# Performance work log

Measured on AMD Instinct MI355X. Metric: run time of the kernel, lower is better.

## Reference

```python
import jax, jax.numpy as jnp
import numpy as np
import math

D_MODEL = 1024
NUM_HEADS = 16
D_K = D_MODEL // NUM_HEADS
B, S = 2, 2048


def setup_inputs() -> dict:
    key = jax.random.key(0)
    ks = jax.random.split(key, 11)
    scale = 1.0 / math.sqrt(D_MODEL)
    inp = {
        "query": jax.random.normal(ks[0], (B, S, D_MODEL), jnp.float32),
        "key": jax.random.normal(ks[1], (B, S, D_MODEL), jnp.float32),
        "value": jax.random.normal(ks[2], (B, S, D_MODEL), jnp.float32),
        "Wq": jax.random.normal(ks[3], (D_MODEL, D_MODEL), jnp.float32) * scale,
        "bq": jnp.zeros((D_MODEL,), jnp.float32),
        "Wk": jax.random.normal(ks[4], (D_MODEL, D_MODEL), jnp.float32) * scale,
        "bk": jnp.zeros((D_MODEL,), jnp.float32),
        "Wv": jax.random.normal(ks[5], (D_MODEL, D_MODEL), jnp.float32) * scale,
        "bv": jnp.zeros((D_MODEL,), jnp.float32),
        "Wo": jax.random.normal(ks[6], (D_MODEL, D_MODEL), jnp.float32) * scale,
        "bo": jnp.zeros((D_MODEL,), jnp.float32),
    }
    return inp


def reference(query, key, value, Wq, bq, Wk, bk, Wv, bv, Wo, bo):
    b, s, _ = query.shape
    # QKV projections (torch Linear: x @ W.T + b)
    Q = query @ Wq.T + bq
    K = key @ Wk.T + bk
    V = value @ Wv.T + bv
    # [b, h, s, d_k]
    Q = Q.reshape(b, s, NUM_HEADS, D_K).transpose(0, 2, 1, 3)
    K = K.reshape(b, s, NUM_HEADS, D_K).transpose(0, 2, 1, 3)
    V = V.reshape(b, s, NUM_HEADS, D_K).transpose(0, 2, 1, 3)
    score = jnp.einsum("bhqd,bhkd->bhqk", Q, K) / math.sqrt(D_K)
    attn = jax.nn.softmax(score, axis=-1)
    out = jnp.einsum("bhqk,bhkd->bhqd", attn, V)
    out = out.transpose(0, 2, 1, 3).reshape(b, s, D_MODEL)
    return out @ Wo.T + bo
```

## Files before the change

### kernel.cpp

```cpp
#include <hip/hip_runtime.h>

#define NHEADS 16
#define SEQ    2048
#define BATCH  2
#define DMODEL 1024
#define MTOT   4096

typedef __attribute__((ext_vector_type(8)))  short short8;
typedef __attribute__((ext_vector_type(4)))  float f32x4;
typedef __attribute__((ext_vector_type(16))) float f32x16;

__device__ __forceinline__ unsigned short f32_to_bf16_rn(float x) {
  unsigned int u = __float_as_uint(x);
  u += 0x7fffu + ((u >> 16) & 1u);
  return (unsigned short)(u >> 16);
}

__device__ __forceinline__ unsigned cvt_pk_bf16(float lo, float hi_) {
  unsigned r;
  asm("v_cvt_pk_bf16_f32 %0, %1, %2" : "=v"(r) : "v"(lo), "v"(hi_));
  return r;
}

__device__ __forceinline__ void permlane32_swap(unsigned &a, unsigned &b) {
  asm("v_permlane32_swap_b32 %0, %1" : "+v"(a), "+v"(b));
}

__device__ __forceinline__ void async16(void* lds, const void* g) {
  __builtin_amdgcn_global_load_lds((const __attribute__((address_space(1))) unsigned int*)g,
                                   (__attribute__((address_space(3))) unsigned int*)lds, 16, 0, 0);
}

__global__ void cvt_bf16_kernel(const float* __restrict__ x0, const float* __restrict__ x1,
                                const float* __restrict__ x2,
                                const float* __restrict__ w0, const float* __restrict__ w1,
                                const float* __restrict__ w2, const float* __restrict__ w3,
                                unsigned short* __restrict__ obase)
{
  const int e = (blockIdx.x*256 + threadIdx.x)*8;
  const float* src;
  int local;
  if (e < 3*4194304) {
    const int t = e >> 22;
    src = t==0 ? x0 : t==1 ? x1 : x2;
    local = e & (4194304-1);
    src += local;
    local += t << 22;
  } else {
    const int f = e - 3*4194304;
    const int t = f >> 20;
    src = t==0 ? w0 : t==1 ? w1 : t==2 ? w2 : w3;
    src += (f & (1048576-1));
    local = e;
  }
  const float4 v0 = *(const float4*)(src);
  const float4 v1 = *(const float4*)(src + 4);
  union { unsigned short u[8]; uint4 v; } r;
  r.u[0] = f32_to_bf16_rn(v0.x); r.u[1] = f32_to_bf16_rn(v0.y);
  r.u[2] = f32_to_bf16_rn(v0.z); r.u[3] = f32_to_bf16_rn(v0.w);
  r.u[4] = f32_to_bf16_rn(v1.x); r.u[5] = f32_to_bf16_rn(v1.y);
  r.u[6] = f32_to_bf16_rn(v1.z); r.u[7] = f32_to_bf16_rn(v1.w);
  *(uint4*)(obase + local) = r.v;
}

template<int BM>
__device__ __forceinline__ void gemm_core(const unsigned short* __restrict__ A,
                                          const unsigned short* __restrict__ W,
                                          unsigned short* sA, unsigned short* sB,
                                          int m0, int n0, f32x4 (&acc)[BM/32][4])
{
  constexpr int MI = BM/32;
  const int t = threadIdx.x;
  const int lane = t & 63;
  const int wv = t >> 6;
  const int wm = wv >> 1, wn = wv & 1;
  const int lr = lane & 15, lk = lane >> 4;

  for (int kt = 0; kt < DMODEL/64; ++kt) {
    #pragma unroll
    for (int g = 0; g < MI; ++g) {
      const int o  = g*4096 + t*16;
      const int so = o ^ (((o >> 7) & 7) << 4);
      const int row = so >> 7, colE = (so & 127) >> 1;
      async16((char*)sA + o, A + (size_t)(m0 + row)*DMODEL + kt*64 + colE);
    }
    #pragma unroll
    for (int g = 0; g < 4; ++g) {
      const int o  = g*4096 + t*16;
      const int so = o ^ (((o >> 7) & 7) << 4);
      const int row = so >> 7, colE = (so & 127) >> 1;
      async16((char*)sB + o, W + (size_t)(n0 + row)*DMODEL + kt*64 + colE);
    }
    __syncthreads();
    #pragma unroll
    for (int ks = 0; ks < 2; ++ks) {
      short8 af[MI], bf[4];
      #pragma unroll
      for (int mi = 0; mi < MI; ++mi) {
        const int row = wm*(BM/2) + mi*16 + lr;
        const int sl  = (ks*4 + lk) ^ (row & 7);
        af[mi] = *(const short8*)(sA + row*64 + sl*8);
      }
      #pragma unroll
      for (int ni = 0; ni < 4; ++ni) {
        const int row = wn*64 + ni*16 + lr;
        const int sl  = (ks*4 + lk) ^ (row & 7);
        bf[ni] = *(const short8*)(sB + row*64 + sl*8);
      }
      #pragma unroll
      for (int mi = 0; mi < MI; ++mi)
        #pragma unroll
        for (int ni = 0; ni < 4; ++ni)
          acc[mi][ni] = __builtin_amdgcn_mfma_f32_16x16x32_bf16(af[mi], bf[ni], acc[mi][ni], 0, 0, 0);
    }
    __syncthreads();
  }
}

__global__ __launch_bounds__(256, 3)
void qkv_gemm_kernel(const unsigned short* __restrict__ Xq, const unsigned short* __restrict__ Xk,
                     const unsigned short* __restrict__ Xv,
                     const unsigned short* __restrict__ Wq, const unsigned short* __restrict__ Wk,
                     const unsigned short* __restrict__ Wv,
                     const float* __restrict__ bq, const float* __restrict__ bk,
                     const float* __restrict__ bv,
                     unsigned short* __restrict__ Qp, unsigned short* __restrict__ Kp,
                     unsigned short* __restrict__ Vtp)
{
  constexpr int BM = 128;
  constexpr int MI = BM/32;
  __shared__ __align__(16) unsigned short smem[17024];
  unsigned short* sA = smem;
  unsigned short* sB = smem + 8192;

  const int m0   = blockIdx.x * BM;
  const int nabs = blockIdx.y * 128;
  const int wsel = nabs >> 10;
  const int n0   = nabs & 1023;
  const unsigned short* A = wsel==0 ? Xq : wsel==1 ? Xk : Xv;
  const unsigned short* W = wsel==0 ? Wq : wsel==1 ? Wk : Wv;
  const float* bias       = wsel==0 ? bq : wsel==1 ? bk : bv;

  f32x4 acc[MI][4];
  #pragma unroll
  for (int mi = 0; mi < MI; ++mi)
    #pragma unroll
    for (int ni = 0; ni < 4; ++ni)
      acc[mi][ni] = {0.f, 0.f, 0.f, 0.f};

  gemm_core<BM>(A, W, sA, sB, m0, n0, acc);

  const int t = threadIdx.x, lane = t & 63, wvx = t >> 6;
  const int wm = wvx >> 1, wn = wvx & 1;
  const int lr = lane & 15, lk = lane >> 4;

  if (wsel == 2) {
    #pragma unroll
    for (int ni = 0; ni < 4; ++ni) {
      const float badd = bias[n0 + wn*64 + ni*16 + lr];
      #pragma unroll
      for (int mi = 0; mi < MI; ++mi)
        #pragma unroll
        for (int r = 0; r < 4; ++r) {
          const int ml = wm*(BM/2) + mi*16 + lk*4 + r;
          smem[(wn*64 + ni*16 + lr)*132 + ml] = f32_to_bf16_rn(acc[mi][ni][r] + badd);
        }
    }
    __syncthreads();
    const int bb = m0 >> 11, s0 = m0 & 2047;
    const int jr = (t & 15)*8, nr = t >> 4;
    #pragma unroll
    for (int pass = 0; pass < 8; ++pass) {
      const int n  = pass*16 + nr;
      const int nn = n0 + n, hh = nn >> 6, d = nn & 63;
      const short8 v = *(const short8*)(smem + n*132 + jr);
      *(short8*)(Vtp + (((size_t)bb*NHEADS + hh)*64 + d)*SEQ + s0 + jr) = v;
    }
  } else {
    unsigned short* dst = wsel==0 ? Qp : Kp;
    const float qscale = (wsel == 0) ? 0.125f * 1.4426950408889634f : 1.0f;
    #pragma unroll
    for (int ni = 0; ni < 4; ++ni) {
      const int nn = n0 + wn*64 + ni*16 + lr;
      const float badd = bias[nn];
      const int hh = nn >> 6, d = nn & 63;
      #pragma unroll
      for (int mi = 0; mi < MI; ++mi) {
        #pragma unroll
        for (int r = 0; r < 4; ++r) {
          const int m = m0 + wm*(BM/2) + mi*16 + lk*4 + r;
          const int bb = m >> 11, s = m & 2047;
          const float v = (acc[mi][ni][r] + badd) * qscale;
          dst[(((size_t)bb*NHEADS + hh)*SEQ + s)*64 + d] = f32_to_bf16_rn(v);
        }
      }
    }
  }
}

__global__ __launch_bounds__(256, 2)
void attn_kernel(const unsigned short* __restrict__ Qp, const unsigned short* __restrict__ Kp,
                 const unsigned short* __restrict__ Vtp,
                 unsigned short* __restrict__ Opar, float* __restrict__ Lpar)
{
  __shared__ __align__(16) unsigned short sm[16384];
  constexpr int NT = 1024/64;

  const int t = threadIdx.x, lane = t & 63, w = t >> 6;
  const int lq = lane & 31, hi = lane >> 5;
  const int f   = blockIdx.x;
  const int wid = (f & 7)*64 + (f >> 3);
  const int qt = wid & 7, h = (wid >> 3) & 15, b = (wid >> 7) & 1, half = (wid >> 8) & 1;

  const size_t bh = (size_t)b*NHEADS + h;
  const unsigned short* Qh = Qp  + bh*SEQ*64;
  const unsigned short* Kh = Kp  + bh*SEQ*64 + (size_t)half*1024*64;
  const unsigned short* Vh = Vtp + bh*64*SEQ;
  const int q0 = qt*256 + w*64;

  short8 qf[2][4];
  #pragma unroll
  for (int qh = 0; qh < 2; ++qh)
    #pragma unroll
    for (int ks = 0; ks < 4; ++ks)
      qf[qh][ks] = *(const short8*)(Qh + (size_t)(q0 + qh*32 + lq)*64 + ks*16 + hi*8);

  f32x16 z16;
  #pragma unroll
  for (int r = 0; r < 16; ++r) z16[r] = 0.f;

  const unsigned short* srcp0;
  size_t sstride;
  if (w < 2) { srcp0 = Kh + (size_t)(w*32 + lq)*64 + hi*8;                      sstride = 64*64; }
  else       { srcp0 = Vh + (size_t)((w-2)*32 + lq)*2048 + half*1024 + hi*8;    sstride = 64;    }

  #pragma unroll
  for (int i = 0; i < 4; ++i)
    async16((char*)sm + w*4096 + i*1024, srcp0 + i*16);

  f32x16 o[2][2];
  float lsa[2][4];
  #pragma unroll
  for (int qh = 0; qh < 2; ++qh) {
    #pragma unroll
    for (int d = 0; d < 2; ++d)
      #pragma unroll
      for (int r = 0; r < 16; ++r) o[qh][d][r] = 0.f;
    #pragma unroll
    for (int j = 0; j < 4; ++j) lsa[qh][j] = 0.f;
  }

  for (int kt = 0; kt < NT; ++kt) {
    {
      const unsigned short* sp = srcp0 + (size_t)((kt + 1) & (NT - 1))*sstride;
      const int nb = ((kt + 1) & 1) * 16384;
      #pragma unroll
      for (int i = 0; i < 4; ++i)
        async16((char*)sm + nb + w*4096 + i*1024, sp + i*16);
    }
    asm volatile("s_waitcnt vmcnt(4)" ::: "memory");
    __builtin_amdgcn_s_barrier();

    const unsigned short* base  = sm + (kt & 1)*8192;
    const unsigned short* vbase = base + 4096;

    f32x16 st[2][2];
    __builtin_amdgcn_s_setprio(1);
    #pragma unroll
    for (int sub = 0; sub < 2; ++sub) {
      #pragma unroll
      for (int ks = 0; ks < 4; ++ks) {
        const short8 kf = *(const short8*)(base + (sub*4 + ks)*512 + lane*8);
        if (ks == 0) {
          st[0][sub] = __builtin_amdgcn_mfma_f32_32x32x16_bf16(kf, qf[0][0], z16, 0, 0, 0);
          st[1][sub] = __builtin_amdgcn_mfma_f32_32x32x16_bf16(kf, qf[1][0], z16, 0, 0, 0);
        } else {
          st[0][sub] = __builtin_amdgcn_mfma_f32_32x32x16_bf16(kf, qf[0][ks], st[0][sub], 0, 0, 0);
          st[1][sub] = __builtin_amdgcn_mfma_f32_32x32x16_bf16(kf, qf[1][ks], st[1][sub], 0, 0, 0);
        }
      }
    }
    __builtin_amdgcn_s_setprio(0);

    unsigned pw[2][2][8];
    #pragma unroll
    for (int qh = 0; qh < 2; ++qh)
      #pragma unroll
      for (int sub = 0; sub < 2; ++sub) {
        #pragma unroll
        for (int r = 0; r < 16; ++r) {
          const float p = __builtin_amdgcn_exp2f(st[qh][sub][r]);
          st[qh][sub][r] = p;
          lsa[qh][r & 3] += p;
        }
        unsigned x0 = cvt_pk_bf16(st[qh][sub][0],  st[qh][sub][1]);
        unsigned x1 = cvt_pk_bf16(st[qh][sub][2],  st[qh][sub][3]);
        unsigned y0 = cvt_pk_bf16(st[qh][sub][4],  st[qh][sub][5]);
        unsigned y1 = cvt_pk_bf16(st[qh][sub][6],  st[qh][sub][7]);
        permlane32_swap(x0, y0);
        permlane32_swap(x1, y1);
        pw[qh][sub][0] = x0; pw[qh][sub][1] = x1; pw[qh][sub][2] = y0; pw[qh][sub][3] = y1;
        unsigned z0 = cvt_pk_bf16(st[qh][sub][8],  st[qh][sub][9]);
        unsigned z1 = cvt_pk_bf16(st[qh][sub][10], st[qh][sub][11]);
        unsigned w0 = cvt_pk_bf16(st[qh][sub][12], st[qh][sub][13]);
        unsigned w1 = cvt_pk_bf16(st[qh][sub][14], st[qh][sub][15]);
        permlane32_swap(z0, w0);
        permlane32_swap(z1, w1);
        pw[qh][sub][4] = z0; pw[qh][sub][5] = z1; pw[qh][sub][6] = w0; pw[qh][sub][7] = w1;
      }

    #pragma unroll
    for (int sub = 0; sub < 2; ++sub) {
      const short8 v00 = *(const short8*)(vbase + (0*4 + 2*sub    )*512 + lane*8);
      const short8 v01 = *(const short8*)(vbase + (0*4 + 2*sub + 1)*512 + lane*8);
      const short8 v10 = *(const short8*)(vbase + (1*4 + 2*sub    )*512 + lane*8);
      const short8 v11 = *(const short8*)(vbase + (1*4 + 2*sub + 1)*512 + lane*8);
      __builtin_amdgcn_s_setprio(1);
      #pragma unroll
      for (int qh = 0; qh < 2; ++qh) {
        union { unsigned u[4]; short8 s; } pA, pB;
        pA.u[0] = pw[qh][sub][0]; pA.u[1] = pw[qh][sub][1];
        pA.u[2] = pw[qh][sub][2]; pA.u[3] = pw[qh][sub][3];
        pB.u[0] = pw[qh][sub][4]; pB.u[1] = pw[qh][sub][5];
        pB.u[2] = pw[qh][sub][6]; pB.u[3] = pw[qh][sub][7];
        o[qh][0] = __builtin_amdgcn_mfma_f32_32x32x16_bf16(v00, pA.s, o[qh][0], 0, 0, 0);
        o[qh][1] = __builtin_amdgcn_mfma_f32_32x32x16_bf16(v10, pA.s, o[qh][1], 0, 0, 0);
        o[qh][0] = __builtin_amdgcn_mfma_f32_32x32x16_bf16(v01, pB.s, o[qh][0], 0, 0, 0);
        o[qh][1] = __builtin_amdgcn_mfma_f32_32x32x16_bf16(v11, pB.s, o[qh][1], 0, 0, 0);
      }
      __builtin_amdgcn_s_setprio(0);
    }
    asm volatile("" ::: "memory");
    __builtin_amdgcn_s_barrier();
  }

  float lsum[2];
  #pragma unroll
  for (int qh = 0; qh < 2; ++qh) {
    lsum[qh] = (lsa[qh][0] + lsa[qh][1]) + (lsa[qh][2] + lsa[qh][3]);
    lsum[qh] += __shfl_xor(lsum[qh], 32);
  }
  if (lane < 32) {
    Lpar[half*65536 + b*32768 + h*2048 + q0 + lq]      = lsum[0];
    Lpar[half*65536 + b*32768 + h*2048 + q0 + 32 + lq] = lsum[1];
  }

  #pragma unroll
  for (int qh = 0; qh < 2; ++qh) {
    const size_t row = (size_t)b*SEQ + q0 + qh*32 + lq;
    unsigned short* orow = Opar + ((size_t)half*MTOT + row)*DMODEL + h*64;
    #pragma unroll
    for (int dblk = 0; dblk < 2; ++dblk)
      #pragma unroll
      for (int g = 0; g < 4; ++g) {
        union { unsigned short us[4]; uint2 v; } pk;
        #pragma unroll
        for (int r = 0; r < 4; ++r) pk.us[r] = f32_to_bf16_rn(o[qh][dblk][g*4 + r]);
        *(uint2*)(orow + dblk*32 + g*8 + hi*4) = pk.v;
      }
  }
}

__global__ void combine_kernel(const unsigned short* __restrict__ Opar,
                               const float* __restrict__ Lpar,
                               unsigned short* __restrict__ Op)
{
  const int flat = blockIdx.x*256 + threadIdx.x;
  const int row  = flat >> 8;
  const int col4 = flat & 255;
  const int b = row >> 11, q = row & 2047, h = col4 >> 4;

  const uint2 a = *(const uint2*)(Opar + (size_t)row*DMODEL + col4*4);
  const uint2 c = *(const uint2*)(Opar + (size_t)(MTOT + row)*DMODEL + col4*4);
  const float l0 = Lpar[b*32768 + h*2048 + q];
  const float l1 = Lpar[65536 + b*32768 + h*2048 + q];
  const float inv = __builtin_amdgcn_rcpf(l0 + l1);

  union { unsigned u[2]; uint2 v; } ua, uc;
  ua.v = a; uc.v = c;
  union { unsigned short us[4]; uint2 v; } out;
  #pragma unroll
  for (int j = 0; j < 4; ++j) {
    const unsigned va = ((j & 1) ? (ua.u[j >> 1] >> 16) : (ua.u[j >> 1] & 0xffffu)) << 16;
    const unsigned vc = ((j & 1) ? (uc.u[j >> 1] >> 16) : (uc.u[j >> 1] & 0xffffu)) << 16;
    const float s = (__uint_as_float(va) + __uint_as_float(vc)) * inv;
    out.us[j] = f32_to_bf16_rn(s);
  }
  *(uint2*)(Op + (size_t)row*DMODEL + col4*4) = out.v;
}

__global__ __launch_bounds__(256, 2)
void oproj_gemm_kernel(const unsigned short* __restrict__ Oin, const unsigned short* __restrict__ Wo,
                       const float* __restrict__ bo, float* __restrict__ out)
{
  constexpr int BM = 64;
  constexpr int MI = BM/32;
  __shared__ __align__(16) unsigned short sA[BM*64];
  __shared__ __align__(16) unsigned short sB[128*64];
  const int m0 = blockIdx.x * BM;
  const int n0 = blockIdx.y * 128;

  f32x4 acc[MI][4];
  #pragma unroll
  for (int mi = 0; mi < MI; ++mi)
    #pragma unroll
    for (int ni = 0; ni < 4; ++ni)
      acc[mi][ni] = {0.f,0.f,0.f,0.f};

  gemm_core<BM>(Oin, Wo, sA, sB, m0, n0, acc);

  const int t = threadIdx.x, lane = t & 63, wvx = t >> 6;
  const int wm = wvx >> 1, wn = wvx & 1;
  const int lr = lane & 15, lk = lane >> 4;

  #pragma unroll
  for (int ni = 0; ni < 4; ++ni) {
    const int nn = n0 + wn*64 + ni*16 + lr;
    const float badd = bo[nn];
    #pragma unroll
    for (int mi = 0; mi < MI; ++mi)
      #pragma unroll
      for (int r = 0; r < 4; ++r) {
        const int m = m0 + wm*(BM/2) + mi*16 + lk*4 + r;
        out[(size_t)m*DMODEL + nn] = acc[mi][ni][r] + badd;
      }
  }
}

extern "C" void kernel_launch(void* const* d_in, const int* in_sizes, int n_in,
                              void* d_out, int out_size, void* d_ws, size_t ws_size,
                              hipStream_t stream) {
  const float* query = (const float*)d_in[0];
  const float* key   = (const float*)d_in[1];
  const float* value = (const float*)d_in[2];
  const float* Wq    = (const float*)d_in[3];
  const float* bq    = (const float*)d_in[4];
  const float* Wk    = (const float*)d_in[5];
  const float* bk    = (const float*)d_in[6];
  const float* Wv    = (const float*)d_in[7];
  const float* bv    = (const float*)d_in[8];
  const float* Wo    = (const float*)d_in[9];
  const float* bo    = (const float*)d_in[10];

  const size_t NX = (size_t)MTOT*DMODEL;
  const size_t NW = (size_t)DMODEL*DMODEL;
  unsigned short* w   = (unsigned short*)d_ws;
  unsigned short* Xq  = w;
  unsigned short* Xk  = Xq  + NX;
  unsigned short* Xv  = Xk  + NX;
  unsigned short* Wqp = Xv  + NX;
  unsigned short* Wkp = Wqp + NW;
  unsigned short* Wvp = Wkp + NW;
  unsigned short* Wop = Wvp + NW;
  unsigned short* Qp  = Wop + NW;
  unsigned short* Kp  = Qp  + NX;
  unsigned short* Vtp = Kp  + NX;
  unsigned short* Opb = Vtp + NX;
  unsigned short* Opar = w;
  float*          Lpar = (float*)(w + 2*NX);

  cvt_bf16_kernel<<<dim3(8192), 256, 0, stream>>>(
      query, key, value, Wq, Wk, Wv, Wo, w);
  qkv_gemm_kernel<<<dim3(32, 24), 256, 0, stream>>>(
      Xq, Xk, Xv, Wqp, Wkp, Wvp, bq, bk, bv, Qp, Kp, Vtp);
  attn_kernel<<<dim3(512), 256, 0, stream>>>(Qp, Kp, Vtp, Opar, Lpar);
  combine_kernel<<<dim3(4096), 256, 0, stream>>>(Opar, Lpar, Opb);
  oproj_gemm_kernel<<<dim3(64, 8), 256, 0, stream>>>(Opb, Wop, bo, (float*)d_out);
}
```

Measured before the change: 118.1 us.

## Fuse split-KV combine into O-projection GEMM A-tile loading; drop setprio

```diff
diff --git a/kernel.cpp b/kernel.cpp
--- a/kernel.cpp
+++ b/kernel.cpp
@@ -265,7 +265,6 @@
     const unsigned short* vbase = base + 4096;
 
     f32x16 st[2][2];
-    __builtin_amdgcn_s_setprio(1);
     #pragma unroll
     for (int sub = 0; sub < 2; ++sub) {
       #pragma unroll
@@ -280,7 +279,6 @@
         }
       }
     }
-    __builtin_amdgcn_s_setprio(0);
 
     unsigned pw[2][2][8];
     #pragma unroll
@@ -315,7 +313,6 @@
       const short8 v01 = *(const short8*)(vbase + (0*4 + 2*sub + 1)*512 + lane*8);
       const short8 v10 = *(const short8*)(vbase + (1*4 + 2*sub    )*512 + lane*8);
       const short8 v11 = *(const short8*)(vbase + (1*4 + 2*sub + 1)*512 + lane*8);
-      __builtin_amdgcn_s_setprio(1);
       #pragma unroll
       for (int qh = 0; qh < 2; ++qh) {
         union { unsigned u[4]; short8 s; } pA, pB;
@@ -328,7 +325,6 @@
         o[qh][0] = __builtin_amdgcn_mfma_f32_32x32x16_bf16(v01, pB.s, o[qh][0], 0, 0, 0);
         o[qh][1] = __builtin_amdgcn_mfma_f32_32x32x16_bf16(v11, pB.s, o[qh][1], 0, 0, 0);
       }
-      __builtin_amdgcn_s_setprio(0);
     }
     asm volatile("" ::: "memory");
     __builtin_amdgcn_s_barrier();
@@ -361,36 +357,9 @@
   }
 }
 
-__global__ void combine_kernel(const unsigned short* __restrict__ Opar,
-                               const float* __restrict__ Lpar,
-                               unsigned short* __restrict__ Op)
-{
-  const int flat = blockIdx.x*256 + threadIdx.x;
-  const int row  = flat >> 8;
-  const int col4 = flat & 255;
-  const int b = row >> 11, q = row & 2047, h = col4 >> 4;
-
-  const uint2 a = *(const uint2*)(Opar + (size_t)row*DMODEL + col4*4);
-  const uint2 c = *(const uint2*)(Opar + (size_t)(MTOT + row)*DMODEL + col4*4);
-  const float l0 = Lpar[b*32768 + h*2048 + q];
-  const float l1 = Lpar[65536 + b*32768 + h*2048 + q];
-  const float inv = __builtin_amdgcn_rcpf(l0 + l1);
-
-  union { unsigned u[2]; uint2 v; } ua, uc;
-  ua.v = a; uc.v = c;
-  union { unsigned short us[4]; uint2 v; } out;
-  #pragma unroll
-  for (int j = 0; j < 4; ++j) {
-    const unsigned va = ((j & 1) ? (ua.u[j >> 1] >> 16) : (ua.u[j >> 1] & 0xffffu)) << 16;
-    const unsigned vc = ((j & 1) ? (uc.u[j >> 1] >> 16) : (uc.u[j >> 1] & 0xffffu)) << 16;
-    const float s = (__uint_as_float(va) + __uint_as_float(vc)) * inv;
-    out.us[j] = f32_to_bf16_rn(s);
-  }
-  *(uint2*)(Op + (size_t)row*DMODEL + col4*4) = out.v;
-}
-
 __global__ __launch_bounds__(256, 2)
-void oproj_gemm_kernel(const unsigned short* __restrict__ Oin, const unsigned short* __restrict__ Wo,
+void oproj_gemm_kernel(const unsigned short* __restrict__ Opar, const float* __restrict__ Lpar,
+                       const unsigned short* __restrict__ Wo,
                        const float* __restrict__ bo, float* __restrict__ out)
 {
   constexpr int BM = 64;
@@ -400,18 +369,72 @@
   const int m0 = blockIdx.x * BM;
   const int n0 = blockIdx.y * 128;
 
-  f32x4 acc[MI][4];
-  #pragma unroll
-  for (int mi = 0; mi < MI; ++mi)
-    #pragma unroll
-    for (int ni = 0; ni < 4; ++ni)
-      acc[mi][ni] = {0.f,0.f,0.f,0.f};
-
-  gemm_core<BM>(Oin, Wo, sA, sB, m0, n0, acc);
-
   const int t = threadIdx.x, lane = t & 63, wvx = t >> 6;
   const int wm = wvx >> 1, wn = wvx & 1;
   const int lr = lane & 15, lk = lane >> 4;
+
+  f32x4 acc[MI][4];
+  #pragma unroll
+  for (int mi = 0; mi < MI; ++mi)
+    #pragma unroll
+    for (int ni = 0; ni < 4; ++ni)
+      acc[mi][ni] = {0.f,0.f,0.f,0.f};
+
+  for (int kt = 0; kt < DMODEL/64; ++kt) {
+    #pragma unroll
+    for (int g = 0; g < MI; ++g) {
+      const int o  = g*4096 + t*16;
+      const int so = o ^ (((o >> 7) & 7) << 4);
+      const int row = so >> 7, colE = (so & 127) >> 1;
+      const int m = m0 + row, bb = m >> 11, q = m & 2047;
+      const uint4 a0 = *(const uint4*)(Opar + (size_t)m*DMODEL + kt*64 + colE);
+      const uint4 a1 = *(const uint4*)(Opar + (size_t)(MTOT + m)*DMODEL + kt*64 + colE);
+      const float l0 = Lpar[bb*32768 + kt*2048 + q];
+      const float l1 = Lpar[65536 + bb*32768 + kt*2048 + q];
+      const float inv = __builtin_amdgcn_rcpf(l0 + l1);
+      union { uint4 v; unsigned u[4]; } ua, ub, rs;
+      ua.v = a0; ub.v = a1;
+      #pragma unroll
+      for (int j = 0; j < 4; ++j) {
+        const float s0 = __uint_as_float((ua.u[j] & 0xffffu) << 16) +
+                         __uint_as_float((ub.u[j] & 0xffffu) << 16);
+        const float s1 = __uint_as_float(ua.u[j] & 0xffff0000u) +
+                         __uint_as_float(ub.u[j] & 0xffff0000u);
+        rs.u[j] = cvt_pk_bf16(s0 * inv, s1 * inv);
+      }
+      *(uint4*)((char*)sA + o) = rs.v;
+    }
+    #pragma unroll
+    for (int g = 0; g < 4; ++g) {
+      const int o  = g*4096 + t*16;
+      const int so = o ^ (((o >> 7) & 7) << 4);
+      const int row = so >> 7, colE = (so & 127) >> 1;
+      async16((char*)sB + o, Wo + (size_t)(n0 + row)*DMODEL + kt*64 + colE);
+    }
+    __syncthreads();
+    #pragma unroll
+    for (int ks = 0; ks < 2; ++ks) {
+      short8 af[MI], bf[4];
+      #pragma unroll
+      for (int mi = 0; mi < MI; ++mi) {
+        const int row = wm*(BM/2) + mi*16 + lr;
+        const int sl  = (ks*4 + lk) ^ (row & 7);
+        af[mi] = *(const short8*)(sA + row*64 + sl*8);
+      }
+      #pragma unroll
+      for (int ni = 0; ni < 4; ++ni) {
+        const int row = wn*64 + ni*16 + lr;
+        const int sl  = (ks*4 + lk) ^ (row & 7);
+        bf[ni] = *(const short8*)(sB + row*64 + sl*8);
+      }
+      #pragma unroll
+      for (int mi = 0; mi < MI; ++mi)
+        #pragma unroll
+        for (int ni = 0; ni < 4; ++ni)
+          acc[mi][ni] = __builtin_amdgcn_mfma_f32_16x16x32_bf16(af[mi], bf[ni], acc[mi][ni], 0, 0, 0);
+    }
+    __syncthreads();
+  }
 
   #pragma unroll
   for (int ni = 0; ni < 4; ++ni) {
@@ -455,7 +478,6 @@
   unsigned short* Qp  = Wop + NW;
   unsigned short* Kp  = Qp  + NX;
   unsigned short* Vtp = Kp  + NX;
-  unsigned short* Opb = Vtp + NX;
   unsigned short* Opar = w;
   float*          Lpar = (float*)(w + 2*NX);
 
@@ -464,6 +486,5 @@
   qkv_gemm_kernel<<<dim3(32, 24), 256, 0, stream>>>(
       Xq, Xk, Xv, Wqp, Wkp, Wvp, bq, bk, bv, Qp, Kp, Vtp);
   attn_kernel<<<dim3(512), 256, 0, stream>>>(Qp, Kp, Vtp, Opar, Lpar);
-  combine_kernel<<<dim3(4096), 256, 0, stream>>>(Opar, Lpar, Opb);
-  oproj_gemm_kernel<<<dim3(64, 8), 256, 0, stream>>>(Opb, Wop, bo, (float*)d_out);
-}
+  oproj_gemm_kernel<<<dim3(64, 8), 256, 0, stream>>>(Opar, Lpar, Wop, bo, (float*)d_out);
+}
```

New measurement: 120.7 us. 2.2% more time.
